# Optimization experiments

Hardware: AMD Instinct MI355X
Metric: run time of the kernel (lower is better)

The kernel has to match this reference:

```python
import jax, jax.numpy as jnp
import numpy as np

# Module config (matches init_kwargs)
DIM = 1024
NUM_HEADS = 16
HEAD_DIM = DIM // NUM_HEADS
SCALE = HEAD_DIM ** -0.5
WINDOW = 256
EXT = WINDOW // 2  # overlap_window=True -> ext_size = window_size // 2

B, N = 4, 4096  # N is a multiple of WINDOW


def setup_inputs() -> dict:
    key = jax.random.key(0)
    ks = jax.random.split(key, 5)
    x = jax.random.normal(ks[0], (B, N, DIM), dtype=jnp.float32)
    # Learned params (trunc-normal std=0.02 in torch; plain normal*0.02 is fine as a stand-in)
    w_qkv = jax.random.normal(ks[1], (3 * DIM, DIM), dtype=jnp.float32) * 0.02
    b_qkv = jnp.zeros((3 * DIM,), dtype=jnp.float32)
    w_proj = jax.random.normal(ks[2], (DIM, DIM), dtype=jnp.float32) * 0.02
    b_proj = jnp.zeros((DIM,), dtype=jnp.float32)
    return {"x": x, "w_qkv": w_qkv, "b_qkv": b_qkv, "w_proj": w_proj, "b_proj": b_proj}


def _local_attention(x, w_qkv, b_qkv, w_proj, b_proj):
    b, n, c = x.shape
    h, hd, w, e = NUM_HEADS, HEAD_DIM, WINDOW, EXT
    g = n // w  # number of windows (n is a multiple of w)
    kw_len = w + 2 * e  # extended window length for keys/values

    # qkv projection and head split: (3, b, h, n, hd)
    qkv = (x @ w_qkv.T + b_qkv).reshape(b, n, 3, h, hd).transpose(2, 0, 3, 1, 4)
    q, k, v = qkv[0], qkv[1], qkv[2]

    # q: non-overlapping windows -> (b, h, g, w, hd)
    qw = q.reshape(b, h, g, w, hd)

    # k, v: pad seq by ext on both sides, then strided overlapping windows
    kp = jnp.pad(k, ((0, 0), (0, 0), (e, e), (0, 0)))
    vp = jnp.pad(v, ((0, 0), (0, 0), (e, e), (0, 0)))
    # window g covers padded positions [g*w, g*w + kw_len)
    idx = jnp.arange(g)[:, None] * w + jnp.arange(kw_len)[None, :]  # (g, kw_len)
    kw = kp[:, :, idx]  # (b, h, g, kw_len, hd)
    vw = vp[:, :, idx]

    # per-window attention
    dots = jnp.einsum('bhgqd,bhgkd->bhgqk', qw, kw) * SCALE  # (b, h, g, w, kw_len)
    # mask out keys that came from the ext padding (out of [0, n) range)
    pos = idx - e  # global key positions per window
    valid = (pos >= 0) & (pos < n)  # (g, kw_len)
    dots = jnp.where(valid[None, None, :, None, :], dots, -jnp.inf)
    attn = jax.nn.softmax(dots, axis=-1)
    out = jnp.einsum('bhgqk,bhgkd->bhgqd', attn, vw)  # (b, h, g, w, hd)

    # merge windows and heads: (b, n, c)
    out = out.reshape(b, h, n, hd).transpose(0, 2, 1, 3).reshape(b, n, c)
    return out @ w_proj.T + b_proj


def reference(x, w_qkv, b_qkv, w_proj, b_proj):
    return _local_attention(x, w_qkv, b_qkv, w_proj, b_proj)
```

## Files before the change

kernel.cpp:

```cpp
#include <hip/hip_runtime.h>


typedef __attribute__((ext_vector_type(8))) short short8;
typedef __attribute__((ext_vector_type(4))) float f32x4;
typedef __attribute__((ext_vector_type(8))) unsigned short ushort8v;
typedef __attribute__((ext_vector_type(4))) unsigned short ushort4v;
typedef __attribute__((ext_vector_type(4))) unsigned int uint4v;
typedef __attribute__((ext_vector_type(4))) _Float16 half4;

#define K_DIM 1024

__device__ __forceinline__ unsigned short f2bf(float f) {
  unsigned int u = __builtin_bit_cast(unsigned int, f);
  u += 0x7FFFu + ((u >> 16) & 1u);
  return (unsigned short)(u >> 16);
}
__device__ __forceinline__ unsigned short f2h(float f) {
  _Float16 h = (_Float16)f;
  return __builtin_bit_cast(unsigned short, h);
}
__device__ __forceinline__ void gload_lds(const unsigned short* g, unsigned short* l) {
  __builtin_amdgcn_global_load_lds((const __attribute__((address_space(1))) void*)g,
                                   (__attribute__((address_space(3))) void*)l, 16, 0, 0);
}

__global__ __launch_bounds__(256) void convf2b(const float* __restrict__ src,
                                               unsigned short* __restrict__ dst, int n4) {
  int i = blockIdx.x * blockDim.x + threadIdx.x;
  if (i >= n4) return;
  f32x4 v = *(const f32x4*)(src + (size_t)i * 4);
  ushort4v o;
  o[0] = f2bf(v[0]); o[1] = f2bf(v[1]); o[2] = f2bf(v[2]); o[3] = f2bf(v[3]);
  *(ushort4v*)(dst + (size_t)i * 4) = o;
}

__device__ __forceinline__ void gemm256_core(const unsigned short* __restrict__ A,
                                             const unsigned short* __restrict__ Bw,
                                             unsigned short* lds,
                                             int m0, int f0, int tid, f32x4 acc[8][4]) {
  const int lane = tid & 63;
  const int w = tid >> 6;
  const int wm = w >> 2, wn = w & 3;
  const int q15 = lane & 15, quad = lane >> 4;
  const int r7 = q15 & 7;

  const unsigned short* Ag = A + (size_t)m0 * K_DIM;
  const unsigned short* Bg = Bw + (size_t)f0 * K_DIM;

  int goff[4];
#pragma unroll
  for (int r = 0; r < 4; ++r) {
    int slot = r * 512 + tid;
    int row = slot >> 3, s = slot & 7;
    goff[r] = row * K_DIM + (s ^ (row & 7)) * 8;
  }

  auto stage_half = [&](int bb, int kk, int hf) {
    if (hf < 2) {
#pragma unroll
      for (int r2 = 0; r2 < 2; ++r2) {
        int r = hf * 2 + r2;
        gload_lds(Ag + goff[r] + kk, lds + bb * 32768 + (r * 512 + w * 64) * 8);
      }
    } else {
#pragma unroll
      for (int r2 = 0; r2 < 2; ++r2) {
        int r = (hf - 2) * 2 + r2;
        gload_lds(Bg + goff[r] + kk, lds + bb * 32768 + 16384 + (r * 512 + w * 64) * 8);
      }
    }
  };

#pragma unroll
  for (int hf = 0; hf < 4; ++hf) stage_half(0, 0, hf);
  stage_half(1, 64, 2);
  stage_half(1, 64, 3);
  asm volatile("s_waitcnt vmcnt(4)" ::: "memory");
  __builtin_amdgcn_s_barrier();

  const int abase = (wm * 128 + q15) * 64;
  const int bbase = 16384 + (wn * 64 + q15) * 64;
  const int sg0 = quad ^ r7;
  const int sg1 = (4 | quad) ^ r7;

  short8 aq[4], bk0[4], bk1[4];

  for (int t = 0; t < 16; ++t) {
    const int b = t & 1;
    const unsigned short* Lb = lds + b * 32768;

#pragma unroll
    for (int i = 0; i < 4; ++i) aq[i] = *(const short8*)&Lb[abase + i * 1024 + sg0 * 8];
#pragma unroll
    for (int j = 0; j < 4; ++j) bk0[j] = *(const short8*)&Lb[bbase + j * 1024 + sg0 * 8];
    if (t <= 14) stage_half(b ^ 1, (t + 1) * 64, 0);
    __builtin_amdgcn_s_barrier();
    asm volatile("s_waitcnt lgkmcnt(0)" ::: "memory");
    __builtin_amdgcn_sched_barrier(0);
    __builtin_amdgcn_s_setprio(1);
#pragma unroll
    for (int i = 0; i < 4; ++i)
#pragma unroll
      for (int j = 0; j < 4; ++j)
        acc[i][j] = __builtin_amdgcn_mfma_f32_16x16x32_bf16(aq[i], bk0[j], acc[i][j], 0, 0, 0);
    __builtin_amdgcn_s_setprio(0);
    __builtin_amdgcn_s_barrier();

#pragma unroll
    for (int i = 0; i < 4; ++i) aq[i] = *(const short8*)&Lb[abase + (i + 4) * 1024 + sg0 * 8];
#pragma unroll
    for (int j = 0; j < 4; ++j) bk1[j] = *(const short8*)&Lb[bbase + j * 1024 + sg1 * 8];
    if (t <= 14) stage_half(b ^ 1, (t + 1) * 64, 1);
    __builtin_amdgcn_s_barrier();
    asm volatile("s_waitcnt lgkmcnt(0)" ::: "memory");
    __builtin_amdgcn_sched_barrier(0);
    __builtin_amdgcn_s_setprio(1);
#pragma unroll
    for (int i = 0; i < 4; ++i)
#pragma unroll
      for (int j = 0; j < 4; ++j)
        acc[i + 4][j] = __builtin_amdgcn_mfma_f32_16x16x32_bf16(aq[i], bk0[j], acc[i + 4][j], 0, 0, 0);
    __builtin_amdgcn_s_setprio(0);
    __builtin_amdgcn_s_barrier();

#pragma unroll
    for (int i = 0; i < 4; ++i) aq[i] = *(const short8*)&Lb[abase + i * 1024 + sg1 * 8];
    if (t <= 13) stage_half(b, (t + 2) * 64, 2);
    __builtin_amdgcn_s_barrier();
    asm volatile("s_waitcnt lgkmcnt(0)" ::: "memory");
    __builtin_amdgcn_sched_barrier(0);
    __builtin_amdgcn_s_setprio(1);
#pragma unroll
    for (int i = 0; i < 4; ++i)
#pragma unroll
      for (int j = 0; j < 4; ++j)
        acc[i][j] = __builtin_amdgcn_mfma_f32_16x16x32_bf16(aq[i], bk1[j], acc[i][j], 0, 0, 0);
    __builtin_amdgcn_s_setprio(0);
    __builtin_amdgcn_s_barrier();

#pragma unroll
    for (int i = 0; i < 4; ++i) aq[i] = *(const short8*)&Lb[abase + (i + 4) * 1024 + sg1 * 8];
    if (t <= 13) stage_half(b, (t + 2) * 64, 3);
    __builtin_amdgcn_s_barrier();
    asm volatile("s_waitcnt lgkmcnt(0)" ::: "memory");
    __builtin_amdgcn_sched_barrier(0);
    __builtin_amdgcn_s_setprio(1);
#pragma unroll
    for (int i = 0; i < 4; ++i)
#pragma unroll
      for (int j = 0; j < 4; ++j)
        acc[i + 4][j] = __builtin_amdgcn_mfma_f32_16x16x32_bf16(aq[i], bk1[j], acc[i + 4][j], 0, 0, 0);
    __builtin_amdgcn_s_setprio(0);
    if (t <= 13)      asm volatile("s_waitcnt vmcnt(4)" ::: "memory");
    else if (t == 14) asm volatile("s_waitcnt vmcnt(0)" ::: "memory");
    __builtin_amdgcn_s_barrier();
  }
}

__global__ __launch_bounds__(512, 2) void gemm_qkv(const unsigned short* __restrict__ A,
                                                   const unsigned short* __restrict__ Bw,
                                                   const float* __restrict__ bias,
                                                   unsigned short* __restrict__ q,
                                                   unsigned short* __restrict__ k,
                                                   unsigned short* __restrict__ v) {
  __shared__ unsigned short lds[65536];
  int bid = blockIdx.x;
  int xcd = bid & 7, idx = bid >> 3;
  int mt = xcd * 8 + (idx & 7);
  int ft = idx >> 3;
  int m0 = mt * 256, f0 = ft * 256;
  int tid = threadIdx.x;
  f32x4 acc[8][4] = {};
  gemm256_core(A, Bw, lds, m0, f0, tid, acc);

  int lane = tid & 63;
  int w = tid >> 6;
  int wm = w >> 2, wn = w & 3;
  int q15 = lane & 15, quad = lane >> 4;
  int which = f0 >> 10;
  unsigned short* dst = (which == 0) ? q : ((which == 1) ? k : v);
  int hh = ((f0 + wn * 64) >> 6) & 15;
  float bj[4];
#pragma unroll
  for (int j = 0; j < 4; ++j) bj[j] = bias[f0 + wn * 64 + j * 16 + q15];
#pragma unroll
  for (int i = 0; i < 8; ++i) {
#pragma unroll
    for (int r = 0; r < 4; ++r) {
      int m = m0 + wm * 128 + i * 16 + quad * 4 + r;
      int bb = m >> 12, n = m & 4095;
      size_t rowb = ((size_t)(bb * 16 + hh) * 4096 + n) * 64;
#pragma unroll
      for (int j = 0; j < 4; ++j) {
        int d = j * 16 + q15;
        float val = acc[i][j][r] + bj[j];
        dst[rowb + d] = (which == 2) ? f2h(val) : f2bf(val);
      }
    }
  }
}

__global__ __launch_bounds__(512, 2) void gemm_proj(const unsigned short* __restrict__ A,
                                                    const unsigned short* __restrict__ Bw,
                                                    const float* __restrict__ bias,
                                                    float* __restrict__ out) {
  __shared__ unsigned short lds[65536];
  int bid = blockIdx.x;
  int xcd = bid & 7, idx = bid >> 3;
  int mt = xcd * 8 + (idx & 7);
  int ft = idx >> 3;
  int m0 = mt * 256, f0 = ft * 256;
  int tid = threadIdx.x;
  f32x4 acc[8][4] = {};
  gemm256_core(A, Bw, lds, m0, f0, tid, acc);

  int lane = tid & 63;
  int w = tid >> 6;
  int wm = w >> 2, wn = w & 3;
  int q15 = lane & 15, quad = lane >> 4;
  float bj[4];
#pragma unroll
  for (int j = 0; j < 4; ++j) bj[j] = bias[f0 + wn * 64 + j * 16 + q15];
#pragma unroll
  for (int i = 0; i < 8; ++i) {
#pragma unroll
    for (int r = 0; r < 4; ++r) {
      int m = m0 + wm * 128 + i * 16 + quad * 4 + r;
      float* orow = out + (size_t)m * 1024 + f0 + wn * 64;
#pragma unroll
      for (int j = 0; j < 4; ++j)
        orow[j * 16 + q15] = acc[i][j][r] + bj[j];
    }
  }
}

__global__ __launch_bounds__(256) void transpose_v(const unsigned short* __restrict__ v,
                                                   unsigned short* __restrict__ vt) {
  __shared__ unsigned short tile[64][72];
  int bid = blockIdx.x;
  int bh = bid >> 6;
  int n0 = (bid & 63) * 64;
  int tid = threadIdx.x;
#pragma unroll
  for (int r = 0; r < 2; ++r) {
    int c = tid + r * 256;
    int row = c >> 3, col8 = (c & 7) * 8;
    uint4v dv = *(const uint4v*)&v[((size_t)bh * 4096 + n0 + row) * 64 + col8];
    *(uint4v*)&tile[row][col8] = dv;
  }
  __syncthreads();
#pragma unroll
  for (int r = 0; r < 2; ++r) {
    int c = tid + r * 256;
    int d = c >> 3, n8 = (c & 7) * 8;
    ushort8v o;
#pragma unroll
    for (int ii = 0; ii < 8; ++ii) o[ii] = tile[n8 + ii][d];
    *(ushort8v*)&vt[((size_t)bh * 64 + d) * 4096 + n0 + n8] = o;
  }
}

__global__ __launch_bounds__(256) void attn3(const unsigned short* __restrict__ Q,
                                             const unsigned short* __restrict__ Kb,
                                             const unsigned short* __restrict__ Vt,
                                             unsigned short* __restrict__ Ao) {
  __shared__ unsigned short lds2[2][8192];

  int bid = blockIdx.x;
  int qb = bid & 63;
  int bh = bid >> 6;
  int b = bh >> 4, h = bh & 15;
  int tid = threadIdx.x, lane = tid & 63, w = tid >> 6;
  int q0 = qb * 64 + w * 16;
  int g = qb >> 2;
  int kst = g * 256 - 128;
  const size_t base = (size_t)bh * 4096 * 64;
  const int q15 = lane & 15, quad = lane >> 4;

  short8 bq[2];
#pragma unroll
  for (int s = 0; s < 2; ++s)
    bq[s] = *(const short8*)&Q[base + (size_t)(q0 + q15) * 64 + s * 32 + quad * 8];

  half4 spk[32];
  float mx = -1e30f;

  auto stageK = [&](int c, int buf) {
    int kb = kst + c * 128;
    kb = min(max(kb, 0), 4096 - 128);
    const unsigned short* Kg = Kb + base + (size_t)kb * 64;
#pragma unroll
    for (int i = 0; i < 4; ++i) {
      int slot = tid + i * 256;
      int row = slot >> 3, s = slot & 7;
      int gs = s ^ (row & 7);
      gload_lds(Kg + (size_t)row * 64 + gs * 8, &lds2[buf][(w * 64 + i * 256) * 8]);
    }
  };

  stageK(0, 0);
#pragma unroll
  for (int c = 0; c < 4; ++c) {
    __syncthreads();
    if (c < 3) stageK(c + 1, (c + 1) & 1);
    const unsigned short* Kc = lds2[c & 1];
    int r7 = q15 & 7;
#pragma unroll
    for (int nt = 0; nt < 8; ++nt) {
      int t = c * 8 + nt;
      int ky = kst + c * 128 + nt * 16;
      bool valid = (ky >= 0) && (ky < 4096);
      if (valid) {
        int sg0 = quad ^ r7;
        const unsigned short* kr = &Kc[(nt * 16 + q15) * 64];
        short8 ak0 = *(const short8*)&kr[sg0 * 8];
        short8 ak1 = *(const short8*)&kr[(sg0 ^ 4) * 8];
        f32x4 sa = {0.f, 0.f, 0.f, 0.f};
        sa = __builtin_amdgcn_mfma_f32_16x16x32_bf16(ak0, bq[0], sa, 0, 0, 0);
        sa = __builtin_amdgcn_mfma_f32_16x16x32_bf16(ak1, bq[1], sa, 0, 0, 0);
        float s0 = sa[0] * 0.125f, s1 = sa[1] * 0.125f;
        float s2 = sa[2] * 0.125f, s3 = sa[3] * 0.125f;
        mx = fmaxf(mx, fmaxf(fmaxf(s0, s1), fmaxf(s2, s3)));
        half4 pk;
        pk[0] = (_Float16)s0; pk[1] = (_Float16)s1;
        pk[2] = (_Float16)s2; pk[3] = (_Float16)s3;
        spk[t] = pk;
      } else {
        spk[t] = (half4){(_Float16)0.f, (_Float16)0.f, (_Float16)0.f, (_Float16)0.f};
      }
    }
  }
  mx = fmaxf(mx, __shfl_xor(mx, 16, 64));
  mx = fmaxf(mx, __shfl_xor(mx, 32, 64));

  auto stageV = [&](int c, int buf) {
    int kb = kst + c * 128;
    kb = min(max(kb, 0), 4096 - 128);
    const unsigned short* Vg = Vt + (size_t)bh * 64 * 4096 + kb;
#pragma unroll
    for (int i = 0; i < 4; ++i) {
      int slot = tid + i * 256;
      int d = slot >> 4, s = slot & 15;
      int gs = s ^ (d & 15);
      gload_lds(Vg + (size_t)d * 4096 + gs * 8, &lds2[buf][(w * 64 + i * 256) * 8]);
    }
  };

  float sum = 0.f;
  f32x4 oacc[4];
#pragma unroll
  for (int dt = 0; dt < 4; ++dt) oacc[dt] = (f32x4){0.f, 0.f, 0.f, 0.f};

  stageV(0, 0);
#pragma unroll
  for (int c = 0; c < 4; ++c) {
    __syncthreads();
    if (c < 3) stageV(c + 1, (c + 1) & 1);
    const unsigned short* Vc = lds2[c & 1];
#pragma unroll
    for (int nt = 0; nt < 8; ++nt) {
      int t = c * 8 + nt;
      int ky = kst + c * 128 + nt * 16;
      bool valid = (ky >= 0) && (ky < 4096);
      if (!valid) continue;
      half4 sp = spk[t];
      float p0 = __expf((float)sp[0] - mx);
      float p1 = __expf((float)sp[1] - mx);
      float p2 = __expf((float)sp[2] - mx);
      float p3 = __expf((float)sp[3] - mx);
      sum += (p0 + p1) + (p2 + p3);
      half4 pk;
      pk[0] = (_Float16)p0; pk[1] = (_Float16)p1;
      pk[2] = (_Float16)p2; pk[3] = (_Float16)p3;
      int sgb = 2 * nt + (quad >> 1);
      int eo = (quad & 1) * 4;
#pragma unroll
      for (int dt = 0; dt < 4; ++dt) {
        int d = dt * 16 + q15;
        half4 bv = *(const half4*)&Vc[d * 128 + ((sgb ^ q15) * 8) + eo];
        oacc[dt] = __builtin_amdgcn_mfma_f32_16x16x16f16(pk, bv, oacc[dt], 0, 0, 0);
      }
    }
  }
  sum += __shfl_xor(sum, 16, 64);
  sum += __shfl_xor(sum, 32, 64);
  float linv = 1.0f / sum;

  float li[4];
#pragma unroll
  for (int r = 0; r < 4; ++r) li[r] = __shfl(linv, quad * 4 + r, 64);
#pragma unroll
  for (int dt = 0; dt < 4; ++dt) {
#pragma unroll
    for (int r = 0; r < 4; ++r) {
      float o = oacc[dt][r] * li[r];
      Ao[(size_t)(b * 4096 + q0 + quad * 4 + r) * 1024 + h * 64 + dt * 16 + q15] = f2bf(o);
    }
  }
}

extern "C" void kernel_launch(void* const* d_in, const int* in_sizes, int n_in,
                              void* d_out, int out_size, void* d_ws, size_t ws_size,
                              hipStream_t stream) {
  const float* x = (const float*)d_in[0];
  const float* w_qkv = (const float*)d_in[1];
  const float* b_qkv = (const float*)d_in[2];
  const float* w_proj = (const float*)d_in[3];
  const float* b_proj = (const float*)d_in[4];
  float* out = (float*)d_out;

  unsigned short* ws = (unsigned short*)d_ws;
  unsigned short* xb = ws;
  unsigned short* wqkvb = ws + 16777216;
  unsigned short* wprojb = ws + 19922944;
  unsigned short* qb = ws + 20971520;
  unsigned short* kb = ws + 37748736;
  unsigned short* vb = ws + 54525952;
  unsigned short* attnb = ws + 71303168;
  unsigned short* vtb = xb;

  convf2b<<<16384, 256, 0, stream>>>(x, xb, 16777216 / 4);
  convf2b<<<3072, 256, 0, stream>>>(w_qkv, wqkvb, 3145728 / 4);
  convf2b<<<1024, 256, 0, stream>>>(w_proj, wprojb, 1048576 / 4);
  gemm_qkv<<<768, 512, 0, stream>>>(xb, wqkvb, b_qkv, qb, kb, vb);
  transpose_v<<<4096, 256, 0, stream>>>(vb, vtb);
  attn3<<<4096, 256, 0, stream>>>(qb, kb, vtb, attnb);
  gemm_proj<<<256, 512, 0, stream>>>(attnb, wprojb, b_proj, out);
}
```

Before: 359.2 us.

## Restructure GEMM mainloop into two phases with fewer barriers and larger fragment loads

Reworks the GEMM k-loop from four quarter-phases, each with its own pair of barriers, into two half-phases. Each half loads all eight A fragments plus both B fragment sets up front, issues two stage_half prefetches together, and waits with partial lgkmcnt counts instead of full drains. The aim is to cut barrier and LDS-wait stalls and give each MFMA burst more work (32 MFMAs instead of 16). In exchange it needs more live VGPRs, which could hurt occupancy at 512x2 launch bounds. The removed barrier between the first and second phase also relies on the hand-tuned waitcnt values staying correct.

```diff
diff --git a/kernel.cpp b/kernel.cpp
--- a/kernel.cpp
+++ b/kernel.cpp
@@ -83,73 +83,44 @@
   const int sg0 = quad ^ r7;
   const int sg1 = (4 | quad) ^ r7;
 
-  short8 aq[4], bk0[4], bk1[4];
-
   for (int t = 0; t < 16; ++t) {
     const int b = t & 1;
     const unsigned short* Lb = lds + b * 32768;
-
-#pragma unroll
-    for (int i = 0; i < 4; ++i) aq[i] = *(const short8*)&Lb[abase + i * 1024 + sg0 * 8];
+    short8 aq[8], bk0[4], bk1[4];
+
+#pragma unroll
+    for (int i = 0; i < 8; ++i) aq[i] = *(const short8*)&Lb[abase + i * 1024 + sg0 * 8];
 #pragma unroll
     for (int j = 0; j < 4; ++j) bk0[j] = *(const short8*)&Lb[bbase + j * 1024 + sg0 * 8];
-    if (t <= 14) stage_half(b ^ 1, (t + 1) * 64, 0);
+    __builtin_amdgcn_sched_barrier(0);
+#pragma unroll
+    for (int j = 0; j < 4; ++j) bk1[j] = *(const short8*)&Lb[bbase + j * 1024 + sg1 * 8];
+    __builtin_amdgcn_sched_barrier(0);
+    if (t <= 14) { stage_half(b ^ 1, (t + 1) * 64, 0); stage_half(b ^ 1, (t + 1) * 64, 1); }
+    asm volatile("s_waitcnt lgkmcnt(4)" ::: "memory");
+    __builtin_amdgcn_sched_barrier(0);
+    __builtin_amdgcn_s_setprio(1);
+#pragma unroll
+    for (int i = 0; i < 8; ++i)
+#pragma unroll
+      for (int j = 0; j < 4; ++j)
+        acc[i][j] = __builtin_amdgcn_mfma_f32_16x16x32_bf16(aq[i], bk0[j], acc[i][j], 0, 0, 0);
+    __builtin_amdgcn_s_setprio(0);
+
+#pragma unroll
+    for (int i = 0; i < 8; ++i) aq[i] = *(const short8*)&Lb[abase + i * 1024 + sg1 * 8];
+    __builtin_amdgcn_sched_barrier(0);
+    asm volatile("s_waitcnt lgkmcnt(8)" ::: "memory");
     __builtin_amdgcn_s_barrier();
+    if (t <= 13) { stage_half(b, (t + 2) * 64, 2); stage_half(b, (t + 2) * 64, 3); }
     asm volatile("s_waitcnt lgkmcnt(0)" ::: "memory");
     __builtin_amdgcn_sched_barrier(0);
     __builtin_amdgcn_s_setprio(1);
 #pragma unroll
-    for (int i = 0; i < 4; ++i)
-#pragma unroll
-      for (int j = 0; j < 4; ++j)
-        acc[i][j] = __builtin_amdgcn_mfma_f32_16x16x32_bf16(aq[i], bk0[j], acc[i][j], 0, 0, 0);
-    __builtin_amdgcn_s_setprio(0);
-    __builtin_amdgcn_s_barrier();
-
-#pragma unroll
-    for (int i = 0; i < 4; ++i) aq[i] = *(const short8*)&Lb[abase + (i + 4) * 1024 + sg0 * 8];
-#pragma unroll
-    for (int j = 0; j < 4; ++j) bk1[j] = *(const short8*)&Lb[bbase + j * 1024 + sg1 * 8];
-    if (t <= 14) stage_half(b ^ 1, (t + 1) * 64, 1);
-    __builtin_amdgcn_s_barrier();
-    asm volatile("s_waitcnt lgkmcnt(0)" ::: "memory");
-    __builtin_amdgcn_sched_barrier(0);
-    __builtin_amdgcn_s_setprio(1);
-#pragma unroll
-    for (int i = 0; i < 4; ++i)
-#pragma unroll
-      for (int j = 0; j < 4; ++j)
-        acc[i + 4][j] = __builtin_amdgcn_mfma_f32_16x16x32_bf16(aq[i], bk0[j], acc[i + 4][j], 0, 0, 0);
-    __builtin_amdgcn_s_setprio(0);
-    __builtin_amdgcn_s_barrier();
-
-#pragma unroll
-    for (int i = 0; i < 4; ++i) aq[i] = *(const short8*)&Lb[abase + i * 1024 + sg1 * 8];
-    if (t <= 13) stage_half(b, (t + 2) * 64, 2);
-    __builtin_amdgcn_s_barrier();
-    asm volatile("s_waitcnt lgkmcnt(0)" ::: "memory");
-    __builtin_amdgcn_sched_barrier(0);
-    __builtin_amdgcn_s_setprio(1);
-#pragma unroll
-    for (int i = 0; i < 4; ++i)
+    for (int i = 0; i < 8; ++i)
 #pragma unroll
       for (int j = 0; j < 4; ++j)
         acc[i][j] = __builtin_amdgcn_mfma_f32_16x16x32_bf16(aq[i], bk1[j], acc[i][j], 0, 0, 0);
-    __builtin_amdgcn_s_setprio(0);
-    __builtin_amdgcn_s_barrier();
-
-#pragma unroll
-    for (int i = 0; i < 4; ++i) aq[i] = *(const short8*)&Lb[abase + (i + 4) * 1024 + sg1 * 8];
-    if (t <= 13) stage_half(b, (t + 2) * 64, 3);
-    __builtin_amdgcn_s_barrier();
-    asm volatile("s_waitcnt lgkmcnt(0)" ::: "memory");
-    __builtin_amdgcn_sched_barrier(0);
-    __builtin_amdgcn_s_setprio(1);
-#pragma unroll
-    for (int i = 0; i < 4; ++i)
-#pragma unroll
-      for (int j = 0; j < 4; ++j)
-        acc[i + 4][j] = __builtin_amdgcn_mfma_f32_16x16x32_bf16(aq[i], bk1[j], acc[i + 4][j], 0, 0, 0);
     __builtin_amdgcn_s_setprio(0);
     if (t <= 13)      asm volatile("s_waitcnt vmcnt(4)" ::: "memory");
     else if (t == 14) asm volatile("s_waitcnt vmcnt(0)" ::: "memory");
```

After: 370.4 us. +3.1%, slower.
